# Optimization experiments

Hardware: AMD Instinct MI355X
Metric: run time of the kernel (lower is better)

Reference implementation:

```python
import jax, jax.numpy as jnp
import numpy as np

B, T, C = 2, 2048, 2048
N_HEAD, N_GROUPS, HEAD_SIZE = 16, 4, 128
Q_PER_KV = N_HEAD // N_GROUPS


def setup_inputs() -> dict:
    key = jax.random.key(0)
    k1, k2, k3 = jax.random.split(key, 3)
    x = jax.random.normal(k1, (B, T, C), dtype=jnp.float32)
    # real RoPE cache: theta_i = 10000^{-2i/d}, cos/sin of shape [T, head_size//2]
    half = HEAD_SIZE // 2
    inv_freq = 1.0 / (10000.0 ** (jnp.arange(0, half, dtype=jnp.float32) / half))
    t = jnp.arange(T, dtype=jnp.float32)
    freqs = t[:, None] * inv_freq[None, :]  # [T, half]
    cos, sin = jnp.cos(freqs), jnp.sin(freqs)
    w_attn = jax.random.normal(k2, (C, (N_HEAD + 2 * N_GROUPS) * HEAD_SIZE), dtype=jnp.float32) * (C ** -0.5)
    w_proj = jax.random.normal(k3, (C, C), dtype=jnp.float32) * (C ** -0.5)
    return {"x": x, "cos": cos, "sin": sin, "w_attn": w_attn, "w_proj": w_proj}


def _apply_rope(x, cos, sin):
    # flash-attn style, interleaved=False: rotate first/second half of rotary dims
    # x: [B, T, H, D], cos/sin: [T, D//2]
    d2 = cos.shape[-1]
    x1, x2 = x[..., :d2], x[..., d2:2 * d2]
    c = cos[None, :, None, :]
    s = sin[None, :, None, :]
    return jnp.concatenate([x1 * c - x2 * s, x1 * s + x2 * c], axis=-1)


def reference(x, cos, sin, w_attn, w_proj):
    Bx, Tx, Cx = x.shape
    qkv = x @ w_attn  # [B, T, (n_head + 2*G)*hs]
    qkv = qkv.reshape(Bx, Tx, N_GROUPS, Q_PER_KV + 2, HEAD_SIZE)
    q = qkv[:, :, :, :Q_PER_KV, :].reshape(Bx, Tx, N_HEAD, HEAD_SIZE)
    k = qkv[:, :, :, Q_PER_KV, :]        # [B, T, G, hs]
    v = qkv[:, :, :, Q_PER_KV + 1, :]    # [B, T, G, hs]
    q = _apply_rope(q, cos, sin)
    k = _apply_rope(k, cos, sin)
    # GQA attention without materializing repeated K/V
    qg = q.reshape(Bx, Tx, N_GROUPS, Q_PER_KV, HEAD_SIZE)
    scale = 1.0 / jnp.sqrt(jnp.float32(HEAD_SIZE))
    scores = jnp.einsum('bqgpd,bkgd->bgpqk', qg, k) * scale  # [B,G,p,T,T]
    attn = jax.nn.softmax(scores, axis=-1)
    y = jnp.einsum('bgpqk,bkgd->bqgpd', attn, v)  # [B,T,G,p,hs]
    y = y.reshape(Bx, Tx, Cx)
    return y @ w_proj
```

## Files before the change

### kernel.cpp

```cpp
#include <hip/hip_runtime.h>
#include <stdint.h>

#define B_ 2
#define T_ 2048
#define C_ 2048
#define NH 16
#define NG 4
#define HS 128

typedef unsigned short u16;
typedef __bf16 bf16_t;
typedef bf16_t bf16x8 __attribute__((ext_vector_type(8)));
typedef float f32x4 __attribute__((ext_vector_type(4)));

__device__ __forceinline__ u16 f2bf(float f) {
    union { float f; uint32_t u; } v; v.f = f;
    uint32_t r = (v.u + 0x7fffu + ((v.u >> 16) & 1u)) >> 16;
    return (u16)r;
}
__device__ __forceinline__ float bf2f(u16 h) {
    union { uint32_t u; float f; } v; v.u = ((uint32_t)h) << 16;
    return v.f;
}

__device__ __forceinline__ void transpose_body(const float* __restrict__ W, u16* __restrict__ Wt,
                                               int K, int N, int bx, int by, float (*tile)[33]) {
    int n0 = bx * 32, k0 = by * 32;
    int tx = threadIdx.x & 31, ty = threadIdx.x >> 5;
#pragma unroll
    for (int i = 0; i < 4; i++) {
        int r = ty + i * 8;
        tile[r][tx] = W[(size_t)(k0 + r) * N + (n0 + tx)];
    }
    __syncthreads();
#pragma unroll
    for (int i = 0; i < 4; i++) {
        int r = ty + i * 8;
        Wt[(size_t)(n0 + r) * K + (k0 + tx)] = f2bf(tile[tx][r]);
    }
}

__global__ void k_prep(const float* __restrict__ x, u16* __restrict__ xb,
                       const float* __restrict__ wa, u16* __restrict__ wat,
                       const float* __restrict__ wp, u16* __restrict__ wpt) {
    __shared__ float tile[32][33];
    int bid = blockIdx.x;
    if (bid < 8192) {
        int i = bid * 256 + threadIdx.x;
        float4 f = ((const float4*)x)[i];
        ushort4 o;
        o.x = f2bf(f.x); o.y = f2bf(f.y); o.z = f2bf(f.z); o.w = f2bf(f.w);
        ((ushort4*)xb)[i] = o;
    } else if (bid < 8192 + 6144) {
        int id = bid - 8192;
        transpose_body(wa, wat, 2048, 3072, id % 96, id / 96, tile);
    } else {
        int id = bid - 14336;
        transpose_body(wp, wpt, 2048, 2048, id % 64, id / 64, tile);
    }
}


#define MIDB { __builtin_amdgcn_s_barrier();                              \
               asm volatile("s_waitcnt lgkmcnt(0)" ::: "memory");         \
               __builtin_amdgcn_sched_barrier(0); }
#define ENDB { __builtin_amdgcn_s_barrier(); }
#define VMW4 { asm volatile("s_waitcnt vmcnt(4)" ::: "memory"); }
#define VMW0 { asm volatile("s_waitcnt vmcnt(0)" ::: "memory"); }

__device__ __forceinline__ void stage_half(const u16* __restrict__ g, int r0, int k0,
                                           u16* l, int tid) {
#pragma unroll
    for (int i = 0; i < 2; i++) {
        int c = tid + i * 512;
        int row = c >> 3, sl = c & 7;
        const u16* ga = g + (size_t)(r0 + row) * 2048 + k0 + (sl ^ (row & 7)) * 8;
        __builtin_amdgcn_global_load_lds((const __attribute__((address_space(1))) void*)ga,
                                         (__attribute__((address_space(3))) void*)(l + c * 8),
                                         16, 0, 0);
    }
}

__device__ __forceinline__ void rd_a(const u16* slot, int mq, int l16, int quad,
                                     bf16x8 (&af)[4][2]) {
#pragma unroll
    for (int mf = 0; mf < 4; mf++) {
        int row = mq * 64 + mf * 16 + l16;
#pragma unroll
        for (int kk = 0; kk < 2; kk++)
            af[mf][kk] = *(const bf16x8*)(slot + row * 64 + ((kk * 4 + quad) ^ (l16 & 7)) * 8);
    }
}

__device__ __forceinline__ void rd_b(const u16* slot, int nq, int wc1, int l16, int quad,
                                     bf16x8 (&bs)[2][2]) {
#pragma unroll
    for (int g = 0; g < 2; g++) {
        int row = wc1 * 64 + (nq * 2 + g) * 16 + l16;
#pragma unroll
        for (int kk = 0; kk < 2; kk++)
            bs[g][kk] = *(const bf16x8*)(slot + row * 64 + ((kk * 4 + quad) ^ (l16 & 7)) * 8);
    }
}

template <int MQ, int NQ>
__device__ __forceinline__ void mm8(f32x4 (&acc)[8][4], const bf16x8 (&af)[4][2],
                                    const bf16x8 (&bs)[2][2]) {
    __builtin_amdgcn_s_setprio(1);
#pragma unroll
    for (int mf = 0; mf < 4; mf++)
#pragma unroll
        for (int g = 0; g < 2; g++)
#pragma unroll
            for (int kk = 0; kk < 2; kk++)
                acc[MQ * 4 + mf][NQ * 2 + g] = __builtin_amdgcn_mfma_f32_16x16x32_bf16(
                    af[mf][kk], bs[g][kk], acc[MQ * 4 + mf][NQ * 2 + g], 0, 0, 0);
    __builtin_amdgcn_s_setprio(0);
}

__global__ __launch_bounds__(512, 2) void k_gemm_qkv(const u16* __restrict__ A,
                                                     const u16* __restrict__ Bt,
                                                     const float* __restrict__ cosb,
                                                     const float* __restrict__ sinb,
                                                     u16* __restrict__ qa,
                                                     u16* __restrict__ ka,
                                                     u16* __restrict__ vt) {
    extern __shared__ __align__(16) u16 sm[];
    const int tid = threadIdx.x;
    const int wave = tid >> 6, lane = tid & 63;
    const int quad = lane >> 4, l16 = lane & 15;
    const int wr = wave >> 2, wc = wave & 3;
    const int m0 = blockIdx.y * 256;
    const int brow = blockIdx.x * 256;

    const u16* As0 = sm + (0 * 2 + wr) * 8192;
    const u16* As1 = sm + (1 * 2 + wr) * 8192;
    const u16* Bs0 = sm + 32768 + (0 * 2 + (wc >> 1)) * 8192;
    const u16* Bs1 = sm + 32768 + (1 * 2 + (wc >> 1)) * 8192;

    f32x4 acc[8][4] = {};
    bf16x8 af[4][2], b0[2][2], b1[2][2];

    stage_half(A,  m0,        0,  sm + 0 * 8192, tid);
    stage_half(A,  m0 + 128,  0,  sm + 1 * 8192, tid);
    stage_half(Bt, brow,       0,  sm + 32768 + 0 * 8192, tid);
    stage_half(Bt, brow + 128, 0,  sm + 32768 + 1 * 8192, tid);
    stage_half(Bt, brow,       64, sm + 32768 + 2 * 8192, tid);
    stage_half(Bt, brow + 128, 64, sm + 32768 + 3 * 8192, tid);
    VMW4;
    __builtin_amdgcn_s_barrier();

    for (int i = 0; i < 15; i++) {
        const int k0 = i * 128;
        rd_a(As0, 0, l16, quad, af); rd_b(Bs0, 0, wc & 1, l16, quad, b0);
        stage_half(A, m0, k0 + 64, sm + 2 * 8192, tid);
        MIDB; mm8<0, 0>(acc, af, b0); ENDB;
        rd_b(Bs0, 1, wc & 1, l16, quad, b1);
        stage_half(A, m0 + 128, k0 + 64, sm + 3 * 8192, tid);
        MIDB; mm8<0, 1>(acc, af, b1); ENDB;
        rd_a(As0, 1, l16, quad, af);
        stage_half(Bt, brow, k0 + 128, sm + 32768 + 0 * 8192, tid);
        MIDB; mm8<1, 1>(acc, af, b1); ENDB;
        stage_half(Bt, brow + 128, k0 + 128, sm + 32768 + 1 * 8192, tid);
        MIDB; mm8<1, 0>(acc, af, b0); VMW4; ENDB;
        rd_a(As1, 0, l16, quad, af); rd_b(Bs1, 0, wc & 1, l16, quad, b0);
        stage_half(A, m0, k0 + 128, sm + 0 * 8192, tid);
        MIDB; mm8<0, 0>(acc, af, b0); ENDB;
        rd_b(Bs1, 1, wc & 1, l16, quad, b1);
        stage_half(A, m0 + 128, k0 + 128, sm + 1 * 8192, tid);
        MIDB; mm8<0, 1>(acc, af, b1); ENDB;
        rd_a(As1, 1, l16, quad, af);
        stage_half(Bt, brow, k0 + 192, sm + 32768 + 2 * 8192, tid);
        MIDB; mm8<1, 1>(acc, af, b1); ENDB;
        stage_half(Bt, brow + 128, k0 + 192, sm + 32768 + 3 * 8192, tid);
        MIDB; mm8<1, 0>(acc, af, b0); VMW4; ENDB;
    }
    {
        rd_a(As0, 0, l16, quad, af); rd_b(Bs0, 0, wc & 1, l16, quad, b0);
        stage_half(A, m0, 1984, sm + 2 * 8192, tid);
        MIDB; mm8<0, 0>(acc, af, b0); ENDB;
        rd_b(Bs0, 1, wc & 1, l16, quad, b1);
        stage_half(A, m0 + 128, 1984, sm + 3 * 8192, tid);
        MIDB; mm8<0, 1>(acc, af, b1); ENDB;
        rd_a(As0, 1, l16, quad, af);
        MIDB; mm8<1, 1>(acc, af, b1); ENDB;
        MIDB; mm8<1, 0>(acc, af, b0); VMW0; ENDB;
        rd_a(As1, 0, l16, quad, af); rd_b(Bs1, 0, wc & 1, l16, quad, b0);
        MIDB; mm8<0, 0>(acc, af, b0); ENDB;
        rd_b(Bs1, 1, wc & 1, l16, quad, b1);
        MIDB; mm8<0, 1>(acc, af, b1); ENDB;
        rd_a(As1, 1, l16, quad, af);
        MIDB; mm8<1, 1>(acc, af, b1); ENDB;
        MIDB; mm8<1, 0>(acc, af, b0); ENDB;
    }

    __syncthreads();
    const int s = blockIdx.x * 2 + (wc >> 1);
    const int stype = s % 6, grp = s / 6;
    const int dhalf = wc & 1;
    const int b = blockIdx.y >> 3;
    const int tb = (blockIdx.y & 7) * 256 + wr * 128;
    const int rid = wr * 2 + (wc >> 1);
    float4* xch = (float4*)sm;

    if (stype < 5 && dhalf == 1) {
#pragma unroll
        for (int mf = 0; mf < 8; mf++)
#pragma unroll
            for (int g = 0; g < 4; g++)
                xch[((rid * 8 + mf) * 4 + g) * 64 + quad * 16 + l16] = *(float4*)&acc[mf][g];
    }
    __syncthreads();
    if (stype < 5) {
        if (dhalf == 0) {
            const float QS = 0.08838834764831845f * 1.44269504088896341f;
            const float sc = (stype < 4) ? QS : 1.0f;
            u16* dst = (stype < 4) ? qa + ((size_t)(b * NH + grp * 4 + stype)) * T_ * 128
                                   : ka + ((size_t)(b * NG + grp)) * T_ * 128;
#pragma unroll
            for (int mf = 0; mf < 8; mf++)
#pragma unroll
                for (int g = 0; g < 4; g++) {
                    float4 x2 = xch[((rid * 8 + mf) * 4 + g) * 64 + quad * 16 + l16];
                    const float* x2p = (const float*)&x2;
                    int d = g * 16 + l16;
#pragma unroll
                    for (int r = 0; r < 4; r++) {
                        int t = tb + mf * 16 + quad * 4 + r;
                        float cc = cosb[t * 64 + d], ss = sinb[t * 64 + d];
                        float x1 = acc[mf][g][r];
                        u16* drow = dst + (size_t)t * 128;
                        drow[d] = f2bf((x1 * cc - x2p[r] * ss) * sc);
                        drow[d + 64] = f2bf((x1 * ss + x2p[r] * cc) * sc);
                    }
                }
        }
    } else {
        size_t vb = ((size_t)(b * NG + grp)) * 128;
#pragma unroll
        for (int mf = 0; mf < 8; mf++)
#pragma unroll
            for (int g = 0; g < 4; g++) {
                int d = dhalf * 64 + g * 16 + l16;
                int t0 = tb + mf * 16 + quad * 4;
                ushort4 o = make_ushort4(f2bf(acc[mf][g][0]), f2bf(acc[mf][g][1]),
                                         f2bf(acc[mf][g][2]), f2bf(acc[mf][g][3]));
                *(ushort4*)(vt + (vb + d) * T_ + t0) = o;
            }
    }
}

__global__ __launch_bounds__(256) void k_gemm_bt(const u16* __restrict__ A,
                                                 const u16* __restrict__ Bt,
                                                 float* __restrict__ C,
                                                 int M, int N, int K) {
    __shared__ __align__(16) u16 As[128 * 32];
    __shared__ __align__(16) u16 Bs[128 * 32];
    const int tid = threadIdx.x;
    const int wave = tid >> 6, lane = tid & 63;
    const int quad = lane >> 4, l16 = lane & 15;
    const int wr = wave >> 1, wc = wave & 1;
    const int m0 = blockIdx.y * 128, n0 = blockIdx.x * 128;

    f32x4 acc[4][4] = {};

    for (int k0 = 0; k0 < K; k0 += 32) {
        __syncthreads();
#pragma unroll
        for (int i = 0; i < 2; i++) {
            int c = tid + i * 256;
            int row = c >> 2, seg = c & 3;
            const u16* ga = A + (size_t)(m0 + row) * K + k0 + seg * 8;
            const u16* gb = Bt + (size_t)(n0 + row) * K + k0 + seg * 8;
            __builtin_amdgcn_global_load_lds((const __attribute__((address_space(1))) void*)ga,
                                             (__attribute__((address_space(3))) void*)&As[c * 8],
                                             16, 0, 0);
            __builtin_amdgcn_global_load_lds((const __attribute__((address_space(1))) void*)gb,
                                             (__attribute__((address_space(3))) void*)&Bs[c * 8],
                                             16, 0, 0);
        }
        __syncthreads();
        bf16x8 a[4], b[4];
#pragma unroll
        for (int mi = 0; mi < 4; mi++)
            a[mi] = *(const bf16x8*)&As[(wr * 64 + mi * 16 + l16) * 32 + quad * 8];
#pragma unroll
        for (int ni = 0; ni < 4; ni++)
            b[ni] = *(const bf16x8*)&Bs[(wc * 64 + ni * 16 + l16) * 32 + quad * 8];
#pragma unroll
        for (int mi = 0; mi < 4; mi++)
#pragma unroll
            for (int ni = 0; ni < 4; ni++)
                acc[mi][ni] = __builtin_amdgcn_mfma_f32_16x16x32_bf16(a[mi], b[ni], acc[mi][ni], 0, 0, 0);
    }
#pragma unroll
    for (int mi = 0; mi < 4; mi++)
#pragma unroll
        for (int ni = 0; ni < 4; ni++)
#pragma unroll
            for (int r = 0; r < 4; r++) {
                int row = m0 + wr * 64 + mi * 16 + quad * 4 + r;
                int col = n0 + wc * 64 + ni * 16 + l16;
                C[(size_t)row * N + col] = acc[mi][ni][r];
            }
}

__global__ __launch_bounds__(256, 2) void k_attn(const u16* __restrict__ qa,
                                                 const u16* __restrict__ ka,
                                                 const u16* __restrict__ vt,
                                                 u16* __restrict__ ya) {
    __shared__ __align__(16) u16 smem[16384];
    u16* Ks = smem;
    u16* Vs = smem + 8192;
    const int tid = threadIdx.x;
    const int wave = tid >> 6, lane = tid & 63;
    const int quad = lane >> 4, l16 = lane & 15;
    const int qt = blockIdx.x, h = blockIdx.y, b = blockIdx.z;
    const int g = h >> 2;

    bf16x8 qf[2][4];
    {
        const u16* qbase = qa + (((size_t)(b * NH + h)) * T_ + qt * 128 + wave * 32 + l16) * 128;
#pragma unroll
        for (int t16 = 0; t16 < 2; t16++)
#pragma unroll
            for (int ks = 0; ks < 4; ks++)
                qf[t16][ks] = *(const bf16x8*)(qbase + t16 * 16 * 128 + ks * 32 + quad * 8);
    }
    const u16* kbase = ka + ((size_t)(b * NG + g)) * T_ * 128;
    const u16* vbase = vt + ((size_t)(b * NG + g)) * 128 * T_;

    f32x4 yacc[2][8] = {};
    float lsum[2] = {0.f, 0.f};

    for (int kt = 0; kt < T_ / 64; kt++) {
        __syncthreads();
#pragma unroll
        for (int i = 0; i < 4; i++) {
            int c = tid + i * 256;
            int row = c >> 4, seg = c & 15;
            *(uint4*)&Ks[row * 128 + (seg ^ (row & 15)) * 8] =
                *(const uint4*)(kbase + (size_t)(kt * 64 + row) * 128 + seg * 8);
        }
#pragma unroll
        for (int i = 0; i < 4; i++) {
            int p = tid + i * 256;
            int d = p >> 3, m = p & 7;
            uint4 dv = *(const uint4*)(vbase + (size_t)d * T_ + kt * 64 + m * 8);
            int segA = (m >> 2) * 4 + (m & 1) * 2;
            int a4 = ((m >> 1) & 1) * 4;
            *(uint2*)&Vs[d * 64 + (segA ^ (d & 7)) * 8 + a4] = make_uint2(dv.x, dv.y);
            *(uint2*)&Vs[d * 64 + ((segA + 1) ^ (d & 7)) * 8 + a4] = make_uint2(dv.z, dv.w);
        }
        __syncthreads();

        f32x4 sacc[2][4] = {};
#pragma unroll
        for (int ks = 0; ks < 4; ks++) {
#pragma unroll
            for (int ni = 0; ni < 4; ni++) {
                bf16x8 kf = *(const bf16x8*)&Ks[(ni * 16 + l16) * 128 + ((ks * 4 + quad) ^ l16) * 8];
                sacc[0][ni] = __builtin_amdgcn_mfma_f32_16x16x32_bf16(kf, qf[0][ks], sacc[0][ni], 0, 0, 0);
                sacc[1][ni] = __builtin_amdgcn_mfma_f32_16x16x32_bf16(kf, qf[1][ks], sacc[1][ni], 0, 0, 0);
            }
        }

        uint32_t pk[2][4][2];
#pragma unroll
        for (int t16 = 0; t16 < 2; t16++) {
#pragma unroll
            for (int ni = 0; ni < 4; ni++) {
                float p0 = exp2f(sacc[t16][ni][0]);
                float p1 = exp2f(sacc[t16][ni][1]);
                float p2 = exp2f(sacc[t16][ni][2]);
                float p3 = exp2f(sacc[t16][ni][3]);
                lsum[t16] += (p0 + p1) + (p2 + p3);
                uint32_t u0 = __float_as_uint(p0) + 0x8000u;
                uint32_t u1 = __float_as_uint(p1) + 0x8000u;
                uint32_t u2 = __float_as_uint(p2) + 0x8000u;
                uint32_t u3 = __float_as_uint(p3) + 0x8000u;
                pk[t16][ni][0] = __builtin_amdgcn_perm(u1, u0, 0x07060302u);
                pk[t16][ni][1] = __builtin_amdgcn_perm(u3, u2, 0x07060302u);
            }
        }

#pragma unroll
        for (int ks2 = 0; ks2 < 2; ks2++) {
            union { uint32_t u[4]; bf16x8 v; } pf0, pf1;
            pf0.u[0] = pk[0][2 * ks2][0];     pf0.u[1] = pk[0][2 * ks2][1];
            pf0.u[2] = pk[0][2 * ks2 + 1][0]; pf0.u[3] = pk[0][2 * ks2 + 1][1];
            pf1.u[0] = pk[1][2 * ks2][0];     pf1.u[1] = pk[1][2 * ks2][1];
            pf1.u[2] = pk[1][2 * ks2 + 1][0]; pf1.u[3] = pk[1][2 * ks2 + 1][1];
#pragma unroll
            for (int tile = 0; tile < 8; tile++) {
                bf16x8 vf = *(const bf16x8*)&Vs[(tile * 16 + l16) * 64 +
                                                ((ks2 * 4 + quad) ^ (l16 & 7)) * 8];
                yacc[0][tile] = __builtin_amdgcn_mfma_f32_16x16x32_bf16(vf, pf0.v, yacc[0][tile], 0, 0, 0);
                yacc[1][tile] = __builtin_amdgcn_mfma_f32_16x16x32_bf16(vf, pf1.v, yacc[1][tile], 0, 0, 0);
            }
        }
    }

#pragma unroll
    for (int t16 = 0; t16 < 2; t16++) {
        lsum[t16] += __shfl_xor(lsum[t16], 16);
        lsum[t16] += __shfl_xor(lsum[t16], 32);
    }

    __syncthreads();
#pragma unroll
    for (int t16 = 0; t16 < 2; t16++) {
        float inv = 1.f / lsum[t16];
        int qrow = wave * 32 + t16 * 16 + l16;
#pragma unroll
        for (int tile = 0; tile < 8; tile++) {
#pragma unroll
            for (int cp = 0; cp < 2; cp++) {
                int d = tile * 16 + quad * 4 + cp * 2;
                uint32_t pv = (uint32_t)f2bf(yacc[t16][tile][cp * 2] * inv) |
                              ((uint32_t)f2bf(yacc[t16][tile][cp * 2 + 1] * inv) << 16);
                *(uint32_t*)&smem[qrow * 128 + ((d >> 3) ^ l16) * 8 + (d & 7)] = pv;
            }
        }
    }
    __syncthreads();
#pragma unroll
    for (int i = 0; i < 8; i++) {
        int cc = tid + i * 256;
        int row = cc >> 4, seg = cc & 15;
        uint4 dv = *(const uint4*)&smem[row * 128 + (seg ^ (row & 15)) * 8];
        size_t q = (size_t)(b * T_ + qt * 128 + row);
        *(uint4*)(ya + q * C_ + h * 128 + seg * 8) = dv;
    }
}

extern "C" void kernel_launch(void* const* d_in, const int* in_sizes, int n_in,
                              void* d_out, int out_size, void* d_ws, size_t ws_size,
                              hipStream_t stream) {
    (void)in_sizes; (void)n_in; (void)out_size; (void)ws_size;
    const float* x = (const float*)d_in[0];
    const float* cosb = (const float*)d_in[1];
    const float* sinb = (const float*)d_in[2];
    const float* w_attn = (const float*)d_in[3];
    const float* w_proj = (const float*)d_in[4];
    float* out = (float*)d_out;

    char* ws = (char*)d_ws;
    size_t off = 0;
    auto alloc = [&](size_t bytes) -> char* {
        char* p = ws + off;
        off += (bytes + 255) & ~(size_t)255;
        return p;
    };
    u16* xb  = (u16*)alloc((size_t)4096 * 2048 * 2);
    u16* wat = (u16*)alloc((size_t)3072 * 2048 * 2);
    u16* wpt = (u16*)alloc((size_t)2048 * 2048 * 2);
    u16* qa  = (u16*)alloc((size_t)B_ * NH * T_ * HS * 2);
    u16* ka  = (u16*)alloc((size_t)B_ * NG * T_ * HS * 2);
    u16* vt  = (u16*)alloc((size_t)B_ * NG * T_ * HS * 2);
    u16* ya  = xb;

    static bool smset = false;
    if (!smset) {
        (void)hipFuncSetAttribute((const void*)k_gemm_qkv,
                                  hipFuncAttributeMaxDynamicSharedMemorySize, 131072);
        smset = true;
    }

    k_prep<<<dim3(18432), dim3(256), 0, stream>>>(x, xb, w_attn, wat, w_proj, wpt);
    k_gemm_qkv<<<dim3(12, 16), dim3(512), 131072, stream>>>(xb, wat, cosb, sinb, qa, ka, vt);
    k_attn<<<dim3(16, 16, 2), dim3(256), 0, stream>>>(qa, ka, vt, ya);
    k_gemm_bt<<<dim3(16, 32), dim3(256), 0, stream>>>(ya, wpt, out, 4096, 2048, 2048);
}
```

Baseline: 314.6 us.

## Double-buffer K/V tiles in attention kernel with async prefetch

The attention kernel now double-buffers K and V in shared memory. K for the next tile goes straight to LDS via global_load_lds, and V for the next tile is prefetched into registers while the current tile's MFMAs run. The per-iteration barrier drops from two to one. It also raises wave priority around the MFMA sections and packs P to bf16 with v_cvt_pk_bf16_f32. The cost is doubled LDS (64KB per block), which may limit occupancy under launch_bounds(256,2), plus extra registers for the V prefetch.

New measurement: 315.8 us. Within noise of the previous version (+0.4%).

```diff
diff --git a/kernel.cpp b/kernel.cpp
--- a/kernel.cpp
+++ b/kernel.cpp
@@ -59,7 +59,6 @@
         transpose_body(wp, wpt, 2048, 2048, id % 64, id / 64, tile);
     }
 }
-
 
 #define MIDB { __builtin_amdgcn_s_barrier();                              \
                asm volatile("s_waitcnt lgkmcnt(0)" ::: "memory");         \
@@ -309,9 +308,7 @@
                                                  const u16* __restrict__ ka,
                                                  const u16* __restrict__ vt,
                                                  u16* __restrict__ ya) {
-    __shared__ __align__(16) u16 smem[16384];
-    u16* Ks = smem;
-    u16* Vs = smem + 8192;
+    __shared__ __align__(16) u16 smem[32768];
     const int tid = threadIdx.x;
     const int wave = tid >> 6, lane = tid & 63;
     const int quad = lane >> 4, l16 = lane & 15;
@@ -332,38 +329,72 @@
 
     f32x4 yacc[2][8] = {};
     float lsum[2] = {0.f, 0.f};
+    uint4 vr[4];
+
+#pragma unroll
+    for (int i = 0; i < 4; i++) {
+        int c = tid + i * 256;
+        int row = c >> 4, seg = c & 15;
+        const u16* gk = kbase + (size_t)row * 128 + (seg ^ (row & 15)) * 8;
+        __builtin_amdgcn_global_load_lds((const __attribute__((address_space(1))) void*)gk,
+                                         (__attribute__((address_space(3))) void*)(smem + c * 8),
+                                         16, 0, 0);
+    }
+#pragma unroll
+    for (int i = 0; i < 4; i++) {
+        int p = tid + i * 256;
+        int d = p >> 3, m = p & 7;
+        vr[i] = *(const uint4*)(vbase + (size_t)d * T_ + m * 8);
+    }
 
     for (int kt = 0; kt < T_ / 64; kt++) {
-        __syncthreads();
-#pragma unroll
-        for (int i = 0; i < 4; i++) {
-            int c = tid + i * 256;
-            int row = c >> 4, seg = c & 15;
-            *(uint4*)&Ks[row * 128 + (seg ^ (row & 15)) * 8] =
-                *(const uint4*)(kbase + (size_t)(kt * 64 + row) * 128 + seg * 8);
-        }
+        const int cur = kt & 1;
+        u16* Kc = smem + cur * 8192;
+        u16* Vc = smem + 16384 + cur * 8192;
+
+        asm volatile("s_waitcnt vmcnt(0)" ::: "memory");
 #pragma unroll
         for (int i = 0; i < 4; i++) {
             int p = tid + i * 256;
             int d = p >> 3, m = p & 7;
-            uint4 dv = *(const uint4*)(vbase + (size_t)d * T_ + kt * 64 + m * 8);
             int segA = (m >> 2) * 4 + (m & 1) * 2;
             int a4 = ((m >> 1) & 1) * 4;
-            *(uint2*)&Vs[d * 64 + (segA ^ (d & 7)) * 8 + a4] = make_uint2(dv.x, dv.y);
-            *(uint2*)&Vs[d * 64 + ((segA + 1) ^ (d & 7)) * 8 + a4] = make_uint2(dv.z, dv.w);
+            *(uint2*)&Vc[d * 64 + (segA ^ (d & 7)) * 8 + a4] = make_uint2(vr[i].x, vr[i].y);
+            *(uint2*)&Vc[d * 64 + ((segA + 1) ^ (d & 7)) * 8 + a4] = make_uint2(vr[i].z, vr[i].w);
         }
         __syncthreads();
 
+        if (kt + 1 < T_ / 64) {
+            u16* Kn = smem + (cur ^ 1) * 8192;
+#pragma unroll
+            for (int i = 0; i < 4; i++) {
+                int c = tid + i * 256;
+                int row = c >> 4, seg = c & 15;
+                const u16* gk = kbase + (size_t)((kt + 1) * 64 + row) * 128 + (seg ^ (row & 15)) * 8;
+                __builtin_amdgcn_global_load_lds((const __attribute__((address_space(1))) void*)gk,
+                                                 (__attribute__((address_space(3))) void*)(Kn + c * 8),
+                                                 16, 0, 0);
+            }
+#pragma unroll
+            for (int i = 0; i < 4; i++) {
+                int p = tid + i * 256;
+                int d = p >> 3, m = p & 7;
+                vr[i] = *(const uint4*)(vbase + (size_t)d * T_ + (kt + 1) * 64 + m * 8);
+            }
+        }
+
         f32x4 sacc[2][4] = {};
+        __builtin_amdgcn_s_setprio(1);
 #pragma unroll
         for (int ks = 0; ks < 4; ks++) {
 #pragma unroll
             for (int ni = 0; ni < 4; ni++) {
-                bf16x8 kf = *(const bf16x8*)&Ks[(ni * 16 + l16) * 128 + ((ks * 4 + quad) ^ l16) * 8];
+                bf16x8 kf = *(const bf16x8*)&Kc[(ni * 16 + l16) * 128 + ((ks * 4 + quad) ^ l16) * 8];
                 sacc[0][ni] = __builtin_amdgcn_mfma_f32_16x16x32_bf16(kf, qf[0][ks], sacc[0][ni], 0, 0, 0);
                 sacc[1][ni] = __builtin_amdgcn_mfma_f32_16x16x32_bf16(kf, qf[1][ks], sacc[1][ni], 0, 0, 0);
             }
         }
+        __builtin_amdgcn_s_setprio(0);
 
         uint32_t pk[2][4][2];
 #pragma unroll
@@ -375,15 +406,12 @@
                 float p2 = exp2f(sacc[t16][ni][2]);
                 float p3 = exp2f(sacc[t16][ni][3]);
                 lsum[t16] += (p0 + p1) + (p2 + p3);
-                uint32_t u0 = __float_as_uint(p0) + 0x8000u;
-                uint32_t u1 = __float_as_uint(p1) + 0x8000u;
-                uint32_t u2 = __float_as_uint(p2) + 0x8000u;
-                uint32_t u3 = __float_as_uint(p3) + 0x8000u;
-                pk[t16][ni][0] = __builtin_amdgcn_perm(u1, u0, 0x07060302u);
-                pk[t16][ni][1] = __builtin_amdgcn_perm(u3, u2, 0x07060302u);
-            }
-        }
-
+                asm("v_cvt_pk_bf16_f32 %0, %1, %2" : "=v"(pk[t16][ni][0]) : "v"(p0), "v"(p1));
+                asm("v_cvt_pk_bf16_f32 %0, %1, %2" : "=v"(pk[t16][ni][1]) : "v"(p2), "v"(p3));
+            }
+        }
+
+        __builtin_amdgcn_s_setprio(1);
 #pragma unroll
         for (int ks2 = 0; ks2 < 2; ks2++) {
             union { uint32_t u[4]; bf16x8 v; } pf0, pf1;
@@ -393,12 +421,13 @@
             pf1.u[2] = pk[1][2 * ks2 + 1][0]; pf1.u[3] = pk[1][2 * ks2 + 1][1];
 #pragma unroll
             for (int tile = 0; tile < 8; tile++) {
-                bf16x8 vf = *(const bf16x8*)&Vs[(tile * 16 + l16) * 64 +
+                bf16x8 vf = *(const bf16x8*)&Vc[(tile * 16 + l16) * 64 +
                                                 ((ks2 * 4 + quad) ^ (l16 & 7)) * 8];
                 yacc[0][tile] = __builtin_amdgcn_mfma_f32_16x16x32_bf16(vf, pf0.v, yacc[0][tile], 0, 0, 0);
                 yacc[1][tile] = __builtin_amdgcn_mfma_f32_16x16x32_bf16(vf, pf1.v, yacc[1][tile], 0, 0, 0);
             }
         }
+        __builtin_amdgcn_s_setprio(0);
     }
 
 #pragma unroll
```
